# Kernel optimization log

Measured on AMD Instinct MI355X. Metric: run time of the kernel, lower is better.

The kernel has to match this reference:

```python
import jax, jax.numpy as jnp
import numpy as np

STAGE_SHAPES = {
    'stage1': [(12, 10, 3, 3), (12, 12, 3, 3), (12, 12, 3, 3)],
    'stage2': [(24, 22, 3, 3), (24, 24, 3, 3), (12, 24, 3, 3)],
    'stage3': [(24, 22, 3, 3), (24, 24, 3, 3), (12, 24, 3, 3)],
    'stage4': [(11, 22, 1, 1)],
}
BN_CH = [12, 12, 12, 24, 24, 12, 24, 24, 12]  # channels of the 9 BN layers, in forward order
OFF = np.concatenate([[0], np.cumsum(BN_CH)]).tolist()
EPS = 1e-5


def _split_weights(wflat, shapes):
    """Slice flat [B, P] hypernet weights into per-layer [B, O, I, k, k] tensors."""
    outs, bg = [], 0
    for s in shapes:
        n = int(np.prod(s))
        outs.append(wflat[:, bg:bg + n].reshape((-1,) + s))
        bg += n
    return outs


def _per_sample_conv(x, w):
    """x: [B, C, H, W], w: [B, O, C, k, k] -> [B, O, H, W]. Each sample uses its own filters (SAME padding = k//2 for odd k)."""
    def one(xi, wi):
        return jax.lax.conv_general_dilated(
            xi[None], wi, window_strides=(1, 1), padding='SAME',
            dimension_numbers=('NCHW', 'OIHW', 'NCHW'))[0]
    return jax.vmap(one)(x, w)


def _bn_eval(y, gamma, beta, mean, var):
    """Eval-mode BatchNorm2d over channel dim of [B, C, H, W]."""
    inv = gamma * jax.lax.rsqrt(var + EPS)
    return y * inv[None, :, None, None] + (beta - mean * inv)[None, :, None, None]


def setup_inputs():
    key = jax.random.key(0)
    ks = jax.random.split(key, 8)
    B, H, W = 64, 128, 128
    x = jax.random.normal(ks[0], (B, 10, H, W), jnp.float32)
    # scale hypernet weights down so 9 stacked convs stay numerically tame
    w_stage1 = jax.random.normal(ks[1], (B, 3672), jnp.float32) * 0.05
    w_stage2 = jax.random.normal(ks[2], (B, 12528), jnp.float32) * 0.05
    w_stage3 = jax.random.normal(ks[3], (B, 12528), jnp.float32) * 0.05
    w_stage4 = jax.random.normal(ks[4], (B, 242), jnp.float32) * 0.05
    n_bn = sum(BN_CH)  # 144
    bn_gamma = jax.random.uniform(ks[5], (n_bn,), jnp.float32, 0.5, 1.5)
    bn_beta = jax.random.normal(ks[6], (n_bn,), jnp.float32) * 0.1
    bn_mean = jnp.zeros((n_bn,), jnp.float32)
    bn_var = jnp.ones((n_bn,), jnp.float32)
    return dict(x=x, w_stage1=w_stage1, w_stage2=w_stage2, w_stage3=w_stage3,
                w_stage4=w_stage4, bn_gamma=bn_gamma, bn_beta=bn_beta,
                bn_mean=bn_mean, bn_var=bn_var)


def reference(x, w_stage1, w_stage2, w_stage3, w_stage4, bn_gamma, bn_beta, bn_mean, bn_var):
    cur = x
    li = 0  # global BN layer index
    for stage_key, wflat in (('stage1', w_stage1), ('stage2', w_stage2), ('stage3', w_stage3)):
        for w in _split_weights(wflat, STAGE_SHAPES[stage_key]):
            conv = _per_sample_conv(cur, w)
            lo, hi = OFF[li], OFF[li + 1]
            bn = _bn_eval(conv, bn_gamma[lo:hi], bn_beta[lo:hi], bn_mean[lo:hi], bn_var[lo:hi])
            cur = jax.nn.relu(bn)
            li += 1
        cur = jnp.concatenate([cur, x], axis=1)  # dense skip: [B, 12+10, H, W]
    w_pred = _split_weights(w_stage4, STAGE_SHAPES['stage4'])[0]  # [B, 11, 22, 1, 1]
    return _per_sample_conv(cur, w_pred)
```

## Files before the change

kernel.cpp:

```cpp
#include <hip/hip_runtime.h>
#include <stdint.h>

#define HW    16384
#define NB    64
#define W2    130
#define PXS   (W2*W2)
#define WQH   70144
#define EPSB  1e-5f
#define PXB   48
#define PROWB (38*PXB)
#define PLH   34656
#define NTH   768
#define NWV   12

typedef _Float16 h8  __attribute__((ext_vector_type(8)));
typedef _Float16 h4  __attribute__((ext_vector_type(4)));
typedef float    f16v __attribute__((ext_vector_type(16)));
typedef float    f4  __attribute__((ext_vector_type(4)));
typedef h8 uh8 __attribute__((aligned(4)));
typedef h4 uh4 __attribute__((aligned(4)));
typedef f4 uf4 __attribute__((aligned(4)));

__global__ void prep_w(const float* __restrict__ w1, const float* __restrict__ w2,
                       const float* __restrict__ w3, const float* __restrict__ w4,
                       const float* __restrict__ g,  const float* __restrict__ be,
                       const float* __restrict__ mu, const float* __restrict__ va,
                       _Float16* __restrict__ wq, float* __restrict__ bias)
{
    const int FO[11]   = {0,576,1152,1728,2880,4032,5184,6336,7488,8640,8768};
    const int start[10]= {0,1080,2376,3672,8424,13608,16200,20952,26136,28728};
    const int COt[10]  = {12,12,12,24,24,12,24,24,12,11};
    const int CIt[10]  = {10,12,12,22,24,24,22,24,24,22};
    const int bnoff[10]= {0,12,24,36,60,84,96,120,144,0};
    const int KST[10]  = {1,1,1,2,2,2,2,2,2,2};

    long tid = (long)blockIdx.x * 256 + threadIdx.x;
    long total = (long)NB * 8768, stride = (long)gridDim.x * 256;
    for (long idx = tid; idx < total; idx += stride) {
        int b = (int)(idx / 8768), i = (int)(idx - (long)b * 8768);
        int l = 9; while (i < FO[l]) --l;
        int j = i - FO[l];
        int f = j >> 6, lane = j & 63;
        int ks = (KST[l] == 2) ? (f & 1) : 0;
        int s  = (KST[l] == 2) ? (f >> 1) : f;
        int co = lane & 31, hi = lane >> 5;
        int CO = COt[l], CI = CIt[l];
        float scale = 1.f;
        if (l < 9 && co < CO) {
            int bi = bnoff[l] + co;
            scale = g[bi] * rsqrtf(va[bi] + EPSB);
        }
        int c0 = ks * 16 + hi * 8;
        __attribute__((aligned(16))) _Float16 vals[8];
#pragma unroll
        for (int e = 0; e < 8; ++e) {
            int c = c0 + e; float wv = 0.f;
            if (co < CO && c < CI) {
                int p = (l < 9) ? start[l] + (co * CI + c) * 9 + s
                                : start[9] + co * CI + c;
                const float* src; long si;
                if      (p <  3672) { src = w1; si = (long)b *  3672 + p; }
                else if (p < 16200) { src = w2; si = (long)b * 12528 + (p -  3672); }
                else if (p < 28728) { src = w3; si = (long)b * 12528 + (p - 16200); }
                else                { src = w4; si = (long)b *   242 + (p - 28728); }
                wv = src[si] * scale;
            }
            vals[e] = (_Float16)wv;
        }
        *(uh8*)(wq + idx * 8) = *(const h8*)vals;
    }
    if (tid < 320) {
        int l = (int)tid >> 5, co = (int)tid & 31;
        float v = 0.f;
        if (l < 9 && co < COt[l]) {
            int bi = bnoff[l] + co;
            float sc = g[bi] * rsqrtf(va[bi] + EPSB);
            v = be[bi] - mu[bi] * sc;
        }
        bias[tid] = v;
    }
}

__global__ void pad_x(const float* __restrict__ x, _Float16* __restrict__ bufA,
                      _Float16* __restrict__ bufB, int b0)
{
    int sl = blockIdx.x >> 3, part = blockIdx.x & 7;
    int gb = b0 + sl;
    const float* __restrict__ xs = x + (long)gb * 10 * HW;
    _Float16* __restrict__ dA = bufA + (long)sl * PXS * 32;
    _Float16* __restrict__ dB = bufB + (long)sl * PXS * 32;
    for (int p = part * 256 + threadIdx.x; p < PXS; p += 2048) {
        int r = p / W2, cc = p - r * W2;
        __attribute__((aligned(16))) _Float16 pxA[32], pxB[32];
#pragma unroll
        for (int i = 0; i < 32; ++i) { pxA[i] = (_Float16)0.f; pxB[i] = (_Float16)0.f; }
        if (r >= 1 && r <= 128 && cc >= 1 && cc <= 128) {
            int so = (r - 1) * 128 + (cc - 1);
#pragma unroll
            for (int c = 0; c < 10; ++c) {
                _Float16 xv = (_Float16)xs[c * HW + so];
                pxA[c] = xv; pxA[12 + c] = xv; pxB[12 + c] = xv;
            }
        }
        _Float16* ap = dA + (long)p * 32;
        _Float16* bp = dB + (long)p * 32;
#pragma unroll
        for (int q = 0; q < 4; ++q) {
            *(uh8*)(ap + q * 8) = *(const h8*)(pxA + q * 8);
            *(uh8*)(bp + q * 8) = *(const h8*)(pxB + q * 8);
        }
    }
}

template<int KST, int NR>
__device__ __forceinline__ void lconv(const char* pin, char* pout,
    const _Float16* wl, const float* __restrict__ bias, int boff,
    int rowStart, int nRows, int colStart, int width,
    int oy0, int ox0, int w, int lo5, int hi)
{
    f4 bv[4];
#pragma unroll
    for (int q = 0; q < 4; ++q) bv[q] = *(const uf4*)(bias + boff + hi * 4 + q * 8);
    constexpr int qmax = (KST == 1) ? 2 : 3;

    const int ncb = (width > 32) ? 2 : 1;
    const int nrg = (nRows + NR - 1) / NR;
    const int nu  = nrg * ncb;
#pragma unroll 1
    for (int u = w; u < nu; u += NWV) {
        int rg, cb;
        if (ncb == 2) { rg = u >> 1; cb = u & 1; } else { rg = u; cb = 0; }
        const int r0   = rowStart + rg * NR;
        const int cs   = cb ? (colStart + width - 32) : colStart;
        const int cmin = cb ? (64 - width) : 0;
        const char* bin = pin + (long)(cs - 1 + lo5) * PXB + hi * 16;

        f16v acc[NR];
        { f16v z = {};
#pragma unroll
          for (int i = 0; i < NR; ++i) acc[i] = z; }

#pragma unroll
        for (int kc = 0; kc < 3; ++kc)
#pragma unroll
        for (int ks = 0; ks < KST; ++ks) {
            h8 bf[NR + 2];
#pragma unroll
            for (int j = 0; j < NR + 2; ++j) {
                int rr = r0 - 1 + j; rr = (rr > 37) ? 37 : rr;
                h8 v = {};
                if (!(ks & hi))
                    v = *(const uh8*)(bin + (long)rr * PROWB + kc * PXB + ks * 32);
                bf[j] = v;
            }
#pragma unroll
            for (int kr = 0; kr < 3; ++kr) {
                h8 af = *(const uh8*)(wl + ((kr * 3 + kc) * KST + ks) * 512);
#pragma unroll
                for (int tt = 0; tt < NR; ++tt)
                    acc[tt] = __builtin_amdgcn_mfma_f32_32x32x16_f16(af, bf[kr + tt], acc[tt], 0, 0, 0);
            }
        }

        const bool cok = (lo5 >= cmin);
        const int  pc  = cs + lo5;
        const int  gx  = ox0 - 3 + pc;
        const bool xin = (unsigned)(gx - 1) < 128u;
#pragma unroll
        for (int tt = 0; tt < NR; ++tt) {
            int pr = r0 + tt;
            if (pr >= rowStart + nRows) continue;
            int gy = oy0 - 3 + pr;
            bool ok = xin && ((unsigned)(gy - 1) < 128u);
            char* po = pout + ((long)pr * 38 + pc) * PXB + hi * 8;
            if (cok) {
#pragma unroll
                for (int q = 0; q < qmax; ++q) {
                    float v0 = ok ? fmaxf(acc[tt][4*q+0] + bv[q][0], 0.f) : 0.f;
                    float v1 = ok ? fmaxf(acc[tt][4*q+1] + bv[q][1], 0.f) : 0.f;
                    float v2 = ok ? fmaxf(acc[tt][4*q+2] + bv[q][2], 0.f) : 0.f;
                    float v3 = ok ? fmaxf(acc[tt][4*q+3] + bv[q][3], 0.f) : 0.f;
                    h4 hv = { (_Float16)v0, (_Float16)v1, (_Float16)v2, (_Float16)v3 };
                    *(uh4*)(po + q * 16) = hv;
                }
            }
        }
    }
}

template<int KST>
__global__ __launch_bounds__(NTH)
void stage3(const _Float16* __restrict__ in, _Float16* __restrict__ out,
            const _Float16* __restrict__ wq, int loff0,
            const float* __restrict__ bias, int boff0, int b0)
{
    __shared__ _Float16 lds[2][PLH];
    const int t = threadIdx.x, w = t >> 6, l = t & 63;
    const int lo5 = l & 31, hi = l >> 5;

    const int nbb = (int)(gridDim.x >> 4);
    int s, tile;
    if ((nbb & 7) == 0) {
        int xcd = (int)(blockIdx.x & 7), j = (int)(blockIdx.x >> 3);
        s = xcd * (nbb >> 3) + (j >> 4); tile = j & 15;
    } else { s = (int)(blockIdx.x >> 4); tile = (int)(blockIdx.x & 15); }
    const int gb  = b0 + s;
    const int oy0 = 1 + (tile >> 2) * 32;
    const int ox0 = 1 + (tile & 3) * 32;

    {
        const char* src = (const char*)(in + (long)s * PXS * 32);
        char* dst = (char*)&lds[0][0];
        h8 stg[6];
#pragma unroll
        for (int k = 0; k < 6; ++k) {
            int idx = k * NTH + t;
            int r = idx / 114, g2 = idx - r * 114;
            int p = g2 / 3,   c  = g2 - p * 3;
            int gy = oy0 - 3 + r, gx = ox0 - 3 + p;
            h8 v = {};
            if (idx < 4332 && (unsigned)gy < 130u && (unsigned)gx < 130u)
                v = *(const uh8*)(src + ((long)gy * W2 + gx) * 64 + c * 16);
            stg[k] = v;
        }
#pragma unroll
        for (int k = 0; k < 6; ++k) {
            int idx = k * NTH + t;
            if (idx < 4332) *(uh8*)(dst + (long)idx * 16) = stg[k];
        }
    }
    __syncthreads();

    const _Float16* wl = wq + (long)gb * WQH + loff0 + (long)l * 8;
    constexpr int LSTEP = 9 * KST * 512;
    lconv<KST,3>((const char*)lds[0], (char*)lds[1], wl,             bias, boff0,      1, 36, 1, 36, oy0, ox0, w, lo5, hi);
    __syncthreads();
    lconv<KST,3>((const char*)lds[1], (char*)lds[0], wl + LSTEP,     bias, boff0 + 32, 2, 34, 2, 34, oy0, ox0, w, lo5, hi);
    __syncthreads();
    lconv<KST,4>((const char*)lds[0], (char*)lds[1], wl + 2 * LSTEP, bias, boff0 + 64, 3, 32, 3, 32, oy0, ox0, w, lo5, hi);
    __syncthreads();

    {
        _Float16* db = out + (long)s * PXS * 32;
        const char* T = (const char*)&lds[1][0];
#pragma unroll
        for (int k = 0; k < 2; ++k) {
            int px = k * NTH + t;
            if (px < 1024) {
                int pr = 3 + (px >> 5), pc = 3 + (px & 31);
                int gy = oy0 + (px >> 5), gx = ox0 + (px & 31);
                const char* sp = T + ((long)pr * 38 + pc) * PXB;
                h8 v0 = *(const uh8*)sp;
                h4 v1 = *(const uh4*)(sp + 16);
                _Float16* dp = db + ((long)gy * W2 + gx) * 32;
                *(uh8*)dp = v0;
                *(uh4*)(dp + 8) = v1;
            }
        }
    }
}

__global__ __launch_bounds__(256, 2)
void conv1(const _Float16* __restrict__ in, float* __restrict__ outF,
           const _Float16* __restrict__ wq, int loff, int b0)
{
    const int s = blockIdx.y, gb = b0 + s;
    const int t = threadIdx.x, w = t >> 6, l = t & 63;
    const int lo5 = l & 31, hi = l >> 5;
    const int cb = blockIdx.x & 3;
    const int y00 = (blockIdx.x >> 2) * 32 + w * 8;
    const int xpix = cb * 32 + lo5;

    const _Float16* wl = wq + (long)gb * WQH + loff + (long)l * 8;
    h8 a0 = *(const uh8*)(wl);
    h8 a1 = *(const uh8*)(wl + 512);
    const _Float16* ib = in + (long)s * PXS * 32;

#pragma unroll 1
    for (int tt = 0; tt < 8; ++tt) {
        int y = y00 + tt;
        const _Float16* bp = ib + ((long)(y + 1) * W2 + xpix + 1) * 32 + hi * 8;
        h8 bA = *(const uh8*)(bp);
        h8 bB = *(const uh8*)(bp + 16);
        f16v acc = {};
        acc = __builtin_amdgcn_mfma_f32_32x32x16_f16(a0, bA, acc, 0, 0, 0);
        acc = __builtin_amdgcn_mfma_f32_32x32x16_f16(a1, bB, acc, 0, 0, 0);
        long px = (long)y * 128 + xpix;
#pragma unroll
        for (int r = 0; r < 16; ++r) {
            int co = (r & 3) + 8 * (r >> 2) + 4 * hi;
            if (co < 11) outF[((long)gb * 11 + co) * HW + px] = acc[r];
        }
    }
}

extern "C" void kernel_launch(void* const* d_in, const int* in_sizes, int n_in,
                              void* d_out, int out_size, void* d_ws, size_t ws_size,
                              hipStream_t stream)
{
    const float *x = (const float*)d_in[0], *w1 = (const float*)d_in[1],
                *w2 = (const float*)d_in[2], *w3 = (const float*)d_in[3],
                *w4 = (const float*)d_in[4], *g  = (const float*)d_in[5],
                *be = (const float*)d_in[6], *mu = (const float*)d_in[7],
                *va = (const float*)d_in[8];
    if (n_in == 9) {
        const float* big801[2] = {nullptr, nullptr}; int n801 = 0;
        const float* bn156[4]  = {nullptr, nullptr, nullptr, nullptr}; int n156 = 0;
        const float *fx = nullptr, *fw1 = nullptr, *fw4 = nullptr;
        for (int i = 0; i < 9; ++i) {
            int sz = in_sizes[i];
            if      (sz == 10485760) fx  = (const float*)d_in[i];
            else if (sz ==   235008) fw1 = (const float*)d_in[i];
            else if (sz ==   801792) { if (n801 < 2) big801[n801++] = (const float*)d_in[i]; }
            else if (sz ==    15488) fw4 = (const float*)d_in[i];
            else if (sz ==      156) { if (n156 < 4) bn156[n156++] = (const float*)d_in[i]; }
        }
        if (fx && fw1 && fw4 && n801 == 2 && n156 == 4) {
            x = fx; w1 = fw1; w2 = big801[0]; w3 = big801[1]; w4 = fw4;
            g = bn156[0]; be = bn156[1]; mu = bn156[2]; va = bn156[3];
        }
    }
    float* out = (float*)d_out;

    const size_t wqB   = (size_t)NB * WQH * 2;
    const size_t biasB = 2048;
    const size_t hdr   = wqB + biasB;
    const size_t perSlot = (size_t)PXS * 128;
    size_t avail = ws_size > hdr ? ws_size - hdr : 0;
    int chunk = (int)(avail / perSlot);
    if (chunk > NB) chunk = NB;
    if (chunk < 1)  chunk = 1;

    _Float16* wq   = (_Float16*)d_ws;
    float*    bias = (float*)((char*)d_ws + wqB);
    _Float16* bufA = (_Float16*)((char*)d_ws + hdr);
    _Float16* bufB = bufA + (size_t)chunk * PXS * 32;

    prep_w<<<2048, 256, 0, stream>>>(w1, w2, w3, w4, g, be, mu, va, wq, bias);

    for (int b0 = 0; b0 < NB; b0 += chunk) {
        int nb = (NB - b0 < chunk) ? (NB - b0) : chunk;
        pad_x<<<nb * 8, 256, 0, stream>>>(x, bufA, bufB, b0);
        int gc = nb * 16;
        dim3 g1(16, nb);
        stage3<1><<<gc, NTH, 0, stream>>>(bufA, bufB, wq,     0, bias,   0, b0);
        stage3<2><<<gc, NTH, 0, stream>>>(bufB, bufA, wq, 13824, bias,  96, b0);
        stage3<2><<<gc, NTH, 0, stream>>>(bufA, bufB, wq, 41472, bias, 192, b0);
        conv1<<<g1, 256, 0, stream>>>(bufB, out, wq, 69120, b0);
    }
}
```

Baseline: 475.9 us.

## Use channel-group-planar LDS layout and double-buffer fragment loads in fused conv

Changes the LDS tile layout from pixel-interleaved (48 bytes per pixel) to channel-group planes of 16 bytes per pixel, so lane reads are contiguous and bank conflicts drop. The conv inner loop now prefetches the next B and A fragments into a second register buffer while the current MFMAs issue, hiding LDS and global latency. The last row groups are clamped to overlap instead of being predicated, and the third layer uses 3-row groups instead of 4. Register pressure goes up with the double buffers, and the overlapping row groups recompute and rewrite a few rows.

```diff
diff --git a/kernel.cpp b/kernel.cpp
--- a/kernel.cpp
+++ b/kernel.cpp
@@ -7,8 +7,9 @@
 #define PXS   (W2*W2)
 #define WQH   70144
 #define EPSB  1e-5f
-#define PXB   48
-#define PROWB (38*PXB)
+#define GP    1444
+#define GPB   23104
+#define ROWB  608
 #define PLH   34656
 #define NTH   768
 #define NWV   12
@@ -118,11 +119,12 @@
     int rowStart, int nRows, int colStart, int width,
     int oy0, int ox0, int w, int lo5, int hi)
 {
-    f4 bv[4];
-#pragma unroll
-    for (int q = 0; q < 4; ++q) bv[q] = *(const uf4*)(bias + boff + hi * 4 + q * 8);
     constexpr int qmax = (KST == 1) ? 2 : 3;
-
+    f4 bv[qmax];
+#pragma unroll
+    for (int q = 0; q < qmax; ++q) bv[q] = *(const uf4*)(bias + boff + hi * 4 + q * 8);
+
+    constexpr int NG = 3 * KST;
     const int ncb = (width > 32) ? 2 : 1;
     const int nrg = (nRows + NR - 1) / NR;
     const int nu  = nrg * ncb;
@@ -130,50 +132,61 @@
     for (int u = w; u < nu; u += NWV) {
         int rg, cb;
         if (ncb == 2) { rg = u >> 1; cb = u & 1; } else { rg = u; cb = 0; }
-        const int r0   = rowStart + rg * NR;
+        int r0 = rowStart + rg * NR;
+        { int rmax = rowStart + nRows - NR; r0 = (r0 > rmax) ? rmax : r0; }
         const int cs   = cb ? (colStart + width - 32) : colStart;
         const int cmin = cb ? (64 - width) : 0;
-        const char* bin = pin + (long)(cs - 1 + lo5) * PXB + hi * 16;
+        const char* bin = pin + (long)hi * GPB
+                        + ((long)(r0 - 1) * 38 + (cs - 1 + lo5)) * 16;
 
         f16v acc[NR];
         { f16v z = {};
 #pragma unroll
           for (int i = 0; i < NR; ++i) acc[i] = z; }
 
-#pragma unroll
-        for (int kc = 0; kc < 3; ++kc)
-#pragma unroll
-        for (int ks = 0; ks < KST; ++ks) {
-            h8 bf[NR + 2];
-#pragma unroll
-            for (int j = 0; j < NR + 2; ++j) {
-                int rr = r0 - 1 + j; rr = (rr > 37) ? 37 : rr;
-                h8 v = {};
-                if (!(ks & hi))
-                    v = *(const uh8*)(bin + (long)rr * PROWB + kc * PXB + ks * 32);
-                bf[j] = v;
-            }
-#pragma unroll
-            for (int kr = 0; kr < 3; ++kr) {
-                h8 af = *(const uh8*)(wl + ((kr * 3 + kc) * KST + ks) * 512);
+        h8 bf[2][NR + 2];
+        h8 af[2][3];
+#pragma unroll
+        for (int j = 0; j < NR + 2; ++j)
+            bf[0][j] = *(const uh8*)(bin + j * ROWB);
+#pragma unroll
+        for (int kr = 0; kr < 3; ++kr)
+            af[0][kr] = *(const uh8*)(wl + (kr * 3 * KST) * 512);
+
+#pragma unroll
+        for (int g = 0; g < NG; ++g) {
+            const int cur = g & 1, nxt = cur ^ 1;
+            if (g + 1 < NG) {
+                const int kc2 = (g + 1) / KST, ks2 = (g + 1) - kc2 * KST;
+#pragma unroll
+                for (int j = 0; j < NR + 2; ++j) {
+                    h8 v = {};
+                    if (!(ks2 & hi))
+                        v = *(const uh8*)(bin + ks2 * 2 * GPB + kc2 * 16 + j * ROWB);
+                    bf[nxt][j] = v;
+                }
+#pragma unroll
+                for (int kr = 0; kr < 3; ++kr)
+                    af[nxt][kr] = *(const uh8*)(wl + ((kr * 3 + kc2) * KST + ks2) * 512);
+            }
+#pragma unroll
+            for (int kr = 0; kr < 3; ++kr)
 #pragma unroll
                 for (int tt = 0; tt < NR; ++tt)
-                    acc[tt] = __builtin_amdgcn_mfma_f32_32x32x16_f16(af, bf[kr + tt], acc[tt], 0, 0, 0);
-            }
+                    acc[tt] = __builtin_amdgcn_mfma_f32_32x32x16_f16(
+                                  af[cur][kr], bf[cur][kr + tt], acc[tt], 0, 0, 0);
         }
 
         const bool cok = (lo5 >= cmin);
         const int  pc  = cs + lo5;
         const int  gx  = ox0 - 3 + pc;
         const bool xin = (unsigned)(gx - 1) < 128u;
-#pragma unroll
-        for (int tt = 0; tt < NR; ++tt) {
-            int pr = r0 + tt;
-            if (pr >= rowStart + nRows) continue;
-            int gy = oy0 - 3 + pr;
-            bool ok = xin && ((unsigned)(gy - 1) < 128u);
-            char* po = pout + ((long)pr * 38 + pc) * PXB + hi * 8;
-            if (cok) {
+        char* pob = pout + (long)hi * 8 + ((long)r0 * 38 + pc) * 16;
+        if (cok) {
+#pragma unroll
+            for (int tt = 0; tt < NR; ++tt) {
+                int gy = oy0 - 3 + r0 + tt;
+                bool ok = xin && ((unsigned)(gy - 1) < 128u);
 #pragma unroll
                 for (int q = 0; q < qmax; ++q) {
                     float v0 = ok ? fmaxf(acc[tt][4*q+0] + bv[q][0], 0.f) : 0.f;
@@ -181,7 +194,7 @@
                     float v2 = ok ? fmaxf(acc[tt][4*q+2] + bv[q][2], 0.f) : 0.f;
                     float v3 = ok ? fmaxf(acc[tt][4*q+3] + bv[q][3], 0.f) : 0.f;
                     h4 hv = { (_Float16)v0, (_Float16)v1, (_Float16)v2, (_Float16)v3 };
-                    *(uh4*)(po + q * 16) = hv;
+                    *(uh4*)(pob + q * GPB + tt * ROWB) = hv;
                 }
             }
         }
@@ -215,18 +228,18 @@
 #pragma unroll
         for (int k = 0; k < 6; ++k) {
             int idx = k * NTH + t;
-            int r = idx / 114, g2 = idx - r * 114;
-            int p = g2 / 3,   c  = g2 - p * 3;
-            int gy = oy0 - 3 + r, gx = ox0 - 3 + p;
+            int g = idx / GP, p = idx - g * GP;
+            int r = p / 38, c = p - r * 38;
+            int gy = oy0 - 3 + r, gx = ox0 - 3 + c;
             h8 v = {};
-            if (idx < 4332 && (unsigned)gy < 130u && (unsigned)gx < 130u)
-                v = *(const uh8*)(src + ((long)gy * W2 + gx) * 64 + c * 16);
+            if (idx < 3 * GP && (unsigned)gy < 130u && (unsigned)gx < 130u)
+                v = *(const uh8*)(src + ((long)gy * W2 + gx) * 64 + g * 16);
             stg[k] = v;
         }
 #pragma unroll
         for (int k = 0; k < 6; ++k) {
             int idx = k * NTH + t;
-            if (idx < 4332) *(uh8*)(dst + (long)idx * 16) = stg[k];
+            if (idx < 3 * GP) *(uh8*)(dst + (long)idx * 16) = stg[k];
         }
     }
     __syncthreads();
@@ -237,7 +250,7 @@
     __syncthreads();
     lconv<KST,3>((const char*)lds[1], (char*)lds[0], wl + LSTEP,     bias, boff0 + 32, 2, 34, 2, 34, oy0, ox0, w, lo5, hi);
     __syncthreads();
-    lconv<KST,4>((const char*)lds[0], (char*)lds[1], wl + 2 * LSTEP, bias, boff0 + 64, 3, 32, 3, 32, oy0, ox0, w, lo5, hi);
+    lconv<KST,3>((const char*)lds[0], (char*)lds[1], wl + 2 * LSTEP, bias, boff0 + 64, 3, 32, 3, 32, oy0, ox0, w, lo5, hi);
     __syncthreads();
 
     {
@@ -249,9 +262,9 @@
             if (px < 1024) {
                 int pr = 3 + (px >> 5), pc = 3 + (px & 31);
                 int gy = oy0 + (px >> 5), gx = ox0 + (px & 31);
-                const char* sp = T + ((long)pr * 38 + pc) * PXB;
+                const char* sp = T + ((long)pr * 38 + pc) * 16;
                 h8 v0 = *(const uh8*)sp;
-                h4 v1 = *(const uh4*)(sp + 16);
+                h4 v1 = *(const uh4*)(sp + GPB);
                 _Float16* dp = db + ((long)gy * W2 + gx) * 32;
                 *(uh8*)dp = v0;
                 *(uh4*)(dp + 8) = v1;
```

After: 537.6 us. 1.13x slower.
